# Optimization experiments

Hardware: AMD Instinct MI355X
Metric: run time of the kernel (lower is better)

The kernel has to match this reference:

```python
import jax, jax.numpy as jnp
import numpy as np

NUM_HEADS = 8
LN_EPS = 1e-5


def layer_norm(x, g, b):
    mu = jnp.mean(x, axis=-1, keepdims=True)
    var = jnp.mean(jnp.square(x - mu), axis=-1, keepdims=True)
    return (x - mu) / jnp.sqrt(var + LN_EPS) * g + b


def setup_inputs() -> dict:
    key = jax.random.key(0)
    ks = jax.random.split(key, 16)
    B, N, D, F = 16, 1024, 256, 1024
    s = 0.02
    return {
        "x": jax.random.normal(ks[0], (B, N, D), jnp.float32),
        "spatial_encoding": jax.random.normal(ks[1], (B, N, N), jnp.float32),
        "edge_encoding": jax.random.normal(ks[2], (B, N, N), jnp.float32),
        "gamma1": jnp.ones((D,), jnp.float32),
        "beta1": jnp.zeros((D,), jnp.float32),
        "gamma2": jnp.ones((D,), jnp.float32),
        "beta2": jnp.zeros((D,), jnp.float32),
        "Wq": jax.random.normal(ks[3], (D, D), jnp.float32) * s,
        "Wk": jax.random.normal(ks[4], (D, D), jnp.float32) * s,
        "Wv": jax.random.normal(ks[5], (D, D), jnp.float32) * s,
        "Wo": jax.random.normal(ks[6], (D, D), jnp.float32) * s,
        "W1": jax.random.normal(ks[7], (F, D), jnp.float32) * s,
        "b1": jnp.zeros((F,), jnp.float32),
        "W2": jax.random.normal(ks[8], (D, F), jnp.float32) * s,
        "b2": jnp.zeros((D,), jnp.float32),
    }


def reference(x, spatial_encoding, edge_encoding, gamma1, beta1, gamma2, beta2,
              Wq, Wk, Wv, Wo, W1, b1, W2, b2):
    B, N, D = x.shape
    H = NUM_HEADS
    hd = D // H
    scale = D ** (-0.5)  # source scales by hidden_dim, not head_size

    att_in = layer_norm(x, gamma1, beta1)

    def proj(W):  # [B,N,D] -> [B,H,N,hd]
        return (att_in @ W.T).reshape(B, N, H, hd).transpose(0, 2, 1, 3)

    q, k, v = proj(Wq), proj(Wk), proj(Wv)
    bias = (spatial_encoding + edge_encoding)[:, None]  # [B,1,N,N]
    a = jnp.einsum('bhnd,bhmd->bhnm', q, k) * scale + bias
    pad_mask = jnp.any(a != 0, axis=-1)  # [B,H,N]
    a = jnp.where(pad_mask[..., None], a, -jnp.inf)
    p = jnp.nan_to_num(jax.nn.softmax(a, axis=-1))
    o = jnp.einsum('bhnm,bhmd->bhnd', p, v)
    attn = o.transpose(0, 2, 1, 3).reshape(B, N, D) @ Wo.T
    att_output = attn + x

    pad_mask2 = jnp.any(att_output == 0, axis=-1)  # [B,N]
    ffn_in = layer_norm(x, gamma2, beta2)  # note: norm of x per the source
    h = jax.nn.gelu(ffn_in @ W1.T + b1, approximate=True)
    ffn_out = h @ W2.T + b2 + att_output
    return jnp.where(pad_mask2[..., None], 0.0, ffn_out)
```

## Files before the change

kernel.cpp:

```cpp
#include <hip/hip_runtime.h>
#include <hip/hip_bf16.h>
#include <math.h>

#define Bq 16
#define Nq 1024
#define Dq 256
#define Fq 1024
#define Hq 8
#define HDq 32
#define Mq (Bq * Nq)
#define SCALE 0.0625f
#define LN_EPS 1e-5f

typedef __attribute__((ext_vector_type(8))) short short8;
typedef __attribute__((ext_vector_type(4))) float f32x4;

__device__ __forceinline__ float bf2f(unsigned short s) {
    unsigned u = ((unsigned)s) << 16;
    return __builtin_bit_cast(float, u);
}
__device__ __forceinline__ unsigned short f2bf(float f) {
    __hip_bfloat16 h = __float2bfloat16(f);
    return __builtin_bit_cast(unsigned short, h);
}

typedef __attribute__((address_space(3))) unsigned int lds_uint;
typedef const __attribute__((address_space(1))) unsigned int glb_uint;
__device__ __forceinline__ void async16(void* lds, const void* g) {
    __builtin_amdgcn_global_load_lds((glb_uint*)g, (lds_uint*)lds, 16, 0, 0);
}

__device__ __forceinline__ float gelu_tanh(float v) {
    const float c = 0.7978845608028654f;
    float u = c * (v + 0.044715f * v * v * v);
    return 0.5f * v * (1.0f + tanhf(u));
}

__global__ __launch_bounds__(256) void cvt_weights(
    const float* __restrict__ Wq, const float* __restrict__ Wk,
    const float* __restrict__ Wv, const float* __restrict__ Wo,
    const float* __restrict__ W1, const float* __restrict__ W2,
    unsigned short* __restrict__ dst)
{
    const int blk = blockIdx.x;
    int seg, local;
    if (blk < 256)      { seg = blk >> 6; local = blk & 63; }
    else if (blk < 512) { seg = 4; local = blk - 256; }
    else                { seg = 5; local = blk - 512; }
    const float* srcs[6] = {Wq, Wk, Wv, Wo, W1, W2};
    const size_t dsto[6] = {0, 65536, 131072, 196608, 262144, 524288};
    const float* src = srcs[seg] + (size_t)local * 1024;
    unsigned short* d = dst + dsto[seg] + (size_t)local * 1024;
    const int t4 = threadIdx.x * 4;
    float4 v = *(const float4*)(src + t4);
    uint2 o;
    o.x = (unsigned)f2bf(v.x) | ((unsigned)f2bf(v.y) << 16);
    o.y = (unsigned)f2bf(v.z) | ((unsigned)f2bf(v.w) << 16);
    *(uint2*)(d + t4) = o;
}

__global__ __launch_bounds__(256) void ln2_kernel(
    const float* __restrict__ x,
    const float* __restrict__ g1, const float* __restrict__ bb1,
    const float* __restrict__ g2, const float* __restrict__ bb2,
    unsigned short* __restrict__ att_in, unsigned short* __restrict__ ffn_in)
{
    const int row = blockIdx.x;
    const int t = threadIdx.x;
    const size_t base = (size_t)row * Dq;
    float v = x[base + t];

    float s = v, sq = v * v;
    #pragma unroll
    for (int off = 32; off > 0; off >>= 1) {
        s  += __shfl_down(s, off);
        sq += __shfl_down(sq, off);
    }
    __shared__ float ssum[4], ssq[4];
    __shared__ float mu_s, rstd_s;
    const int lane = t & 63, wid = t >> 6;
    if (lane == 0) { ssum[wid] = s; ssq[wid] = sq; }
    __syncthreads();
    if (t == 0) {
        float S = ssum[0] + ssum[1] + ssum[2] + ssum[3];
        float Q = ssq[0] + ssq[1] + ssq[2] + ssq[3];
        float mu = S * (1.0f / Dq);
        float var = Q * (1.0f / Dq) - mu * mu;
        mu_s = mu;
        rstd_s = rsqrtf(var + LN_EPS);
    }
    __syncthreads();
    const float nx = (v - mu_s) * rstd_s;
    att_in[base + t] = f2bf(nx * g1[t] + bb1[t]);
    ffn_in[base + t] = f2bf(nx * g2[t] + bb2[t]);
}

#define TM 128
#define TN 128
#define TK 32

__global__ __launch_bounds__(256) void gemm_mfma(
    const unsigned short* __restrict__ A, const unsigned short* __restrict__ W,
    const float* __restrict__ bias, const float* __restrict__ add,
    float* __restrict__ outF, unsigned short* __restrict__ outBF,
    unsigned short* __restrict__ Qb, unsigned short* __restrict__ Kb,
    unsigned short* __restrict__ Vt,
    int M, int Nc, int K, int mode, int apply_gelu)
{
    __shared__ unsigned short As[TM * TK];
    __shared__ unsigned short Bs[TN * TK];
    const int t = threadIdx.x;
    const int w = t >> 6, lane = t & 63;
    const int col = lane & 15, quad = lane >> 4;
    const int wr = w >> 1, wc = w & 1;
    const int row0 = blockIdx.y * TM;
    const int col0 = blockIdx.x * TN;

    f32x4 acc[4][4] = {};

    for (int k0 = 0; k0 < K; k0 += TK) {
        #pragma unroll
        for (int j = 0; j < 2; j++) {
            const int c = w * 128 + j * 64 + lane;
            const int r = c >> 2, seg = c & 3;
            async16(&As[(size_t)(w * 128 + j * 64) * 8],
                    A + (size_t)(row0 + r) * K + k0 + seg * 8);
            async16(&Bs[(size_t)(w * 128 + j * 64) * 8],
                    W + (size_t)(col0 + r) * K + k0 + seg * 8);
        }
        __syncthreads();
        short8 wf[4], af[4];
        #pragma unroll
        for (int i = 0; i < 4; i++)
            wf[i] = *(const short8*)&Bs[(wc * 64 + i * 16 + col) * TK + quad * 8];
        #pragma unroll
        for (int j = 0; j < 4; j++)
            af[j] = *(const short8*)&As[(wr * 64 + j * 16 + col) * TK + quad * 8];
        #pragma unroll
        for (int i = 0; i < 4; i++)
            #pragma unroll
            for (int j = 0; j < 4; j++)
                acc[i][j] = __builtin_amdgcn_mfma_f32_16x16x32_bf16(wf[i], af[j], acc[i][j], 0, 0, 0);
        __syncthreads();
    }

    #pragma unroll
    for (int i = 0; i < 4; i++) {
        #pragma unroll
        for (int j = 0; j < 4; j++) {
            const int c0 = col0 + wc * 64 + i * 16 + quad * 4;
            const int r  = row0 + wr * 64 + j * 16 + col;
            float4 v = make_float4(acc[i][j][0], acc[i][j][1], acc[i][j][2], acc[i][j][3]);
            if (mode == 2 && c0 < 256) { v.x *= SCALE; v.y *= SCALE; v.z *= SCALE; v.w *= SCALE; }
            if (bias) {
                float4 bb = *(const float4*)&bias[c0];
                v.x += bb.x; v.y += bb.y; v.z += bb.z; v.w += bb.w;
            }
            if (apply_gelu) {
                v.x = gelu_tanh(v.x); v.y = gelu_tanh(v.y);
                v.z = gelu_tanh(v.z); v.w = gelu_tanh(v.w);
            }
            if (add) {
                float4 aa = *(const float4*)&add[(size_t)r * Nc + c0];
                v.x += aa.x; v.y += aa.y; v.z += aa.z; v.w += aa.w;
            }
            if (mode == 0) {
                *(float4*)&outF[(size_t)r * Nc + c0] = v;
            } else if (mode == 1) {
                uint2 o;
                o.x = (unsigned)f2bf(v.x) | ((unsigned)f2bf(v.y) << 16);
                o.y = (unsigned)f2bf(v.z) | ((unsigned)f2bf(v.w) << 16);
                *(uint2*)&outBF[(size_t)r * Nc + c0] = o;
            } else {
                const int b = r >> 10, n = r & 1023;
                if (c0 < 512) {
                    const int cq = c0 & 255;
                    const int h = cq >> 5, d0 = cq & 31;
                    unsigned short* dst = (c0 < 256 ? Qb : Kb);
                    uint2 o;
                    o.x = (unsigned)f2bf(v.x) | ((unsigned)f2bf(v.y) << 16);
                    o.y = (unsigned)f2bf(v.z) | ((unsigned)f2bf(v.w) << 16);
                    *(uint2*)&dst[(((size_t)(b * Hq + h) << 10) + n) * HDq + d0] = o;
                } else {
                    const int cv = c0 - 512;
                    const int h = cv >> 5, d0 = cv & 31;
                    unsigned short* dst = Vt + (((size_t)(b * Hq + h) * HDq + d0) << 10) + n;
                    dst[0]      = f2bf(v.x);
                    dst[1024]   = f2bf(v.y);
                    dst[2048]   = f2bf(v.z);
                    dst[3072]   = f2bf(v.w);
                }
            }
        }
    }
}

#define BSTR 1028

__global__ __launch_bounds__(512, 4) void attn_mfma(
    const unsigned short* __restrict__ Qbf, const unsigned short* __restrict__ Kbf,
    const unsigned short* __restrict__ Vt, const float* __restrict__ sp,
    const float* __restrict__ ed, unsigned short* __restrict__ O16)
{
    const int b = blockIdx.y;
    const int n0 = blockIdx.x * 16;
    const int t = threadIdx.x;
    const int h = t >> 6;
    const int lane = t & 63;
    const int col = lane & 15;
    const int quad = lane >> 4;

    __shared__ unsigned short bias16[16 * BSTR];
    __shared__ unsigned short S16[8][16 * 128];

    {
        const float* spb = sp + ((size_t)b * Nq + n0) * Nq;
        const float* edb = ed + ((size_t)b * Nq + n0) * Nq;
        for (int i = t; i < 4096; i += 512) {
            const int r = i >> 8;
            const int c4 = i & 255;
            float4 a = *(const float4*)(spb + (size_t)r * Nq + c4 * 4);
            float4 e = *(const float4*)(edb + (size_t)r * Nq + c4 * 4);
            uint2 o;
            o.x = (unsigned)f2bf(a.x + e.x) | ((unsigned)f2bf(a.y + e.y) << 16);
            o.y = (unsigned)f2bf(a.z + e.z) | ((unsigned)f2bf(a.w + e.w) << 16);
            *(uint2*)&bias16[r * BSTR + c4 * 4] = o;
        }
    }
    __syncthreads();

    const size_t hb = (size_t)b * Hq + h;
    const unsigned short* Qh = Qbf + hb * (Nq * HDq);
    const unsigned short* Kh = Kbf + hb * (Nq * HDq);
    const unsigned short* Vh = Vt  + hb * (HDq * Nq);
    unsigned short* Sw = &S16[h][0];

    const short8 aq = *(const short8*)(Qh + (size_t)(n0 + col) * HDq + quad * 8);

    f32x4 o0 = {0.f, 0.f, 0.f, 0.f}, o1 = {0.f, 0.f, 0.f, 0.f};
    float rsum[4] = {0.f, 0.f, 0.f, 0.f};

    for (int tt = 0; tt < 8; tt++) {
        const int k0 = tt * 128;
        #pragma unroll
        for (int m = 0; m < 8; m++) {
            const int m0 = k0 + m * 16;
            short8 bk = *(const short8*)(Kh + (size_t)(m0 + col) * HDq + quad * 8);
            f32x4 cc = {0.f, 0.f, 0.f, 0.f};
            cc = __builtin_amdgcn_mfma_f32_16x16x32_bf16(aq, bk, cc, 0, 0, 0);
            #pragma unroll
            for (int i = 0; i < 4; i++) {
                const int r = quad * 4 + i;
                float s = cc[i] + bf2f(bias16[r * BSTR + m0 + col]);
                float e = __expf(s);
                rsum[i] += e;
                const int sidx = (r * 128 + m * 16 + col) ^ ((r & 7) << 3);
                Sw[sidx] = f2bf(e);
            }
        }
        #pragma unroll
        for (int c = 0; c < 4; c++) {
            const int ridx = (col * 128 + c * 32 + quad * 8) ^ ((col & 7) << 3);
            short8 ap  = *(const short8*)&Sw[ridx];
            short8 bv0 = *(const short8*)(Vh + (size_t)col * Nq + k0 + c * 32 + quad * 8);
            short8 bv1 = *(const short8*)(Vh + (size_t)(col + 16) * Nq + k0 + c * 32 + quad * 8);
            o0 = __builtin_amdgcn_mfma_f32_16x16x32_bf16(ap, bv0, o0, 0, 0, 0);
            o1 = __builtin_amdgcn_mfma_f32_16x16x32_bf16(ap, bv1, o1, 0, 0, 0);
        }
    }

    #pragma unroll
    for (int off = 1; off < 16; off <<= 1) {
        #pragma unroll
        for (int i = 0; i < 4; i++) rsum[i] += __shfl_xor(rsum[i], off, 16);
    }

    unsigned short* op = O16 + ((size_t)b * Nq + n0) * Dq + h * HDq;
    #pragma unroll
    for (int i = 0; i < 4; i++) {
        const float inv = 1.0f / rsum[i];
        const int q = quad * 4 + i;
        op[(size_t)q * Dq + col]      = f2bf(o0[i] * inv);
        op[(size_t)q * Dq + col + 16] = f2bf(o1[i] * inv);
    }
}

__global__ __launch_bounds__(256) void pad2_kernel(
    const float* __restrict__ AO, float* __restrict__ out)
{
    const int row = blockIdx.x;
    const int t = threadIdx.x;
    const float v = AO[(size_t)row * Dq + t];
    unsigned long long m = __ballot(v == 0.0f);
    __shared__ unsigned long long w[4];
    if ((t & 63) == 0) w[t >> 6] = m;
    __syncthreads();
    if ((w[0] | w[1] | w[2] | w[3]) != 0ULL)
        out[(size_t)row * Dq + t] = 0.0f;
}

extern "C" void kernel_launch(void* const* d_in, const int* in_sizes, int n_in,
                              void* d_out, int out_size, void* d_ws, size_t ws_size,
                              hipStream_t stream)
{
    const float* x      = (const float*)d_in[0];
    const float* sp     = (const float*)d_in[1];
    const float* ed     = (const float*)d_in[2];
    const float* gamma1 = (const float*)d_in[3];
    const float* beta1  = (const float*)d_in[4];
    const float* gamma2 = (const float*)d_in[5];
    const float* beta2  = (const float*)d_in[6];
    const float* Wq     = (const float*)d_in[7];
    const float* Wk     = (const float*)d_in[8];
    const float* Wv     = (const float*)d_in[9];
    const float* Wo     = (const float*)d_in[10];
    const float* W1     = (const float*)d_in[11];
    const float* b1     = (const float*)d_in[12];
    const float* W2     = (const float*)d_in[13];
    const float* b2     = (const float*)d_in[14];
    float* out = (float*)d_out;

    unsigned short* s = (unsigned short*)d_ws;
    const size_t MD = (size_t)Mq * Dq;
    unsigned short* att_in16 = s;
    unsigned short* ffn_in16 = s + MD;
    unsigned short* Qbf      = s + 2 * MD;
    unsigned short* Kbf      = s + 3 * MD;
    unsigned short* Vtb      = s + 4 * MD;
    unsigned short* W16      = s + 5 * MD;
    unsigned short* h16      = s + 5 * MD + 786432;
    unsigned short* O16      = att_in16;
    float*          AO       = (float*)Qbf;

    unsigned short* Wo16 = W16 + 196608;
    unsigned short* W116 = W16 + 262144;
    unsigned short* W216 = W16 + 524288;

    cvt_weights<<<768, 256, 0, stream>>>(Wq, Wk, Wv, Wo, W1, W2, W16);

    ln2_kernel<<<Mq, 256, 0, stream>>>(x, gamma1, beta1, gamma2, beta2, att_in16, ffn_in16);

    dim3 gQKV(768 / TN, Mq / TM);
    gemm_mfma<<<gQKV, 256, 0, stream>>>(att_in16, W16, nullptr, nullptr, nullptr, nullptr,
                                        Qbf, Kbf, Vtb, Mq, 768, Dq, 2, 0);

    attn_mfma<<<dim3(Nq / 16, Bq), 512, 0, stream>>>(Qbf, Kbf, Vtb, sp, ed, O16);

    dim3 gP(Dq / TN, Mq / TM);
    gemm_mfma<<<gP, 256, 0, stream>>>(O16, Wo16, nullptr, x, AO, nullptr,
                                      nullptr, nullptr, nullptr, Mq, Dq, Dq, 0, 0);

    dim3 gF1(Fq / TN, Mq / TM);
    gemm_mfma<<<gF1, 256, 0, stream>>>(ffn_in16, W116, b1, nullptr, nullptr, h16,
                                       nullptr, nullptr, nullptr, Mq, Fq, Dq, 1, 1);

    gemm_mfma<<<gP, 256, 0, stream>>>(h16, W216, b2, AO, out, nullptr,
                                      nullptr, nullptr, nullptr, Mq, Dq, Fq, 0, 0);

    pad2_kernel<<<Mq, 256, 0, stream>>>(AO, out);
}
```

Before: 412.1 us.

## Precompute bf16 attention bias in separate kernel, read from global in attention

Moves the spatial+edge bias sum and bf16 conversion out of the attention kernel into a standalone elementwise kernel that writes a bf16 bias buffer, reusing the h16 workspace. The attention kernel drops its 32KB shared-memory bias tile and the barrier, reads bias directly from global memory per MFMA tile, and raises launch bounds to 8 blocks per CU. This aims to raise occupancy and overlap bias loads with compute. In exchange it adds a full extra write and read of a 32MB bf16 bias tensor and uses strided per-element global loads in the inner loop.

```diff
diff --git a/kernel.cpp b/kernel.cpp
--- a/kernel.cpp
+++ b/kernel.cpp
@@ -57,6 +57,23 @@
     o.x = (unsigned)f2bf(v.x) | ((unsigned)f2bf(v.y) << 16);
     o.y = (unsigned)f2bf(v.z) | ((unsigned)f2bf(v.w) << 16);
     *(uint2*)(d + t4) = o;
+}
+
+__global__ __launch_bounds__(256) void bias_cvt(
+    const float* __restrict__ sp, const float* __restrict__ ed,
+    unsigned short* __restrict__ dst)
+{
+    const size_t i = ((size_t)blockIdx.x * 256 + threadIdx.x) * 8;
+    float4 a0 = *(const float4*)(sp + i);
+    float4 a1 = *(const float4*)(sp + i + 4);
+    float4 e0 = *(const float4*)(ed + i);
+    float4 e1 = *(const float4*)(ed + i + 4);
+    uint4 o;
+    o.x = (unsigned)f2bf(a0.x + e0.x) | ((unsigned)f2bf(a0.y + e0.y) << 16);
+    o.y = (unsigned)f2bf(a0.z + e0.z) | ((unsigned)f2bf(a0.w + e0.w) << 16);
+    o.z = (unsigned)f2bf(a1.x + e1.x) | ((unsigned)f2bf(a1.y + e1.y) << 16);
+    o.w = (unsigned)f2bf(a1.z + e1.z) | ((unsigned)f2bf(a1.w + e1.w) << 16);
+    *(uint4*)(dst + i) = o;
 }
 
 __global__ __launch_bounds__(256) void ln2_kernel(
@@ -195,12 +212,10 @@
     }
 }
 
-#define BSTR 1028
-
-__global__ __launch_bounds__(512, 4) void attn_mfma(
+__global__ __launch_bounds__(512, 8) void attn_mfma(
     const unsigned short* __restrict__ Qbf, const unsigned short* __restrict__ Kbf,
-    const unsigned short* __restrict__ Vt, const float* __restrict__ sp,
-    const float* __restrict__ ed, unsigned short* __restrict__ O16)
+    const unsigned short* __restrict__ Vt, const unsigned short* __restrict__ biasg,
+    unsigned short* __restrict__ O16)
 {
     const int b = blockIdx.y;
     const int n0 = blockIdx.x * 16;
@@ -210,29 +225,13 @@
     const int col = lane & 15;
     const int quad = lane >> 4;
 
-    __shared__ unsigned short bias16[16 * BSTR];
     __shared__ unsigned short S16[8][16 * 128];
-
-    {
-        const float* spb = sp + ((size_t)b * Nq + n0) * Nq;
-        const float* edb = ed + ((size_t)b * Nq + n0) * Nq;
-        for (int i = t; i < 4096; i += 512) {
-            const int r = i >> 8;
-            const int c4 = i & 255;
-            float4 a = *(const float4*)(spb + (size_t)r * Nq + c4 * 4);
-            float4 e = *(const float4*)(edb + (size_t)r * Nq + c4 * 4);
-            uint2 o;
-            o.x = (unsigned)f2bf(a.x + e.x) | ((unsigned)f2bf(a.y + e.y) << 16);
-            o.y = (unsigned)f2bf(a.z + e.z) | ((unsigned)f2bf(a.w + e.w) << 16);
-            *(uint2*)&bias16[r * BSTR + c4 * 4] = o;
-        }
-    }
-    __syncthreads();
 
     const size_t hb = (size_t)b * Hq + h;
     const unsigned short* Qh = Qbf + hb * (Nq * HDq);
     const unsigned short* Kh = Kbf + hb * (Nq * HDq);
     const unsigned short* Vh = Vt  + hb * (HDq * Nq);
+    const unsigned short* bg = biasg + (((size_t)b * Nq + n0) << 10);
     unsigned short* Sw = &S16[h][0];
 
     const short8 aq = *(const short8*)(Qh + (size_t)(n0 + col) * HDq + quad * 8);
@@ -251,7 +250,7 @@
             #pragma unroll
             for (int i = 0; i < 4; i++) {
                 const int r = quad * 4 + i;
-                float s = cc[i] + bf2f(bias16[r * BSTR + m0 + col]);
+                float s = cc[i] + bf2f(bg[(size_t)r * Nq + m0 + col]);
                 float e = __expf(s);
                 rsum[i] += e;
                 const int sidx = (r * 128 + m * 16 + col) ^ ((r & 7) << 3);
@@ -331,6 +330,7 @@
     unsigned short* h16      = s + 5 * MD + 786432;
     unsigned short* O16      = att_in16;
     float*          AO       = (float*)Qbf;
+    unsigned short* bias16   = h16;
 
     unsigned short* Wo16 = W16 + 196608;
     unsigned short* W116 = W16 + 262144;
@@ -338,13 +338,15 @@
 
     cvt_weights<<<768, 256, 0, stream>>>(Wq, Wk, Wv, Wo, W1, W2, W16);
 
+    bias_cvt<<<8192, 256, 0, stream>>>(sp, ed, bias16);
+
     ln2_kernel<<<Mq, 256, 0, stream>>>(x, gamma1, beta1, gamma2, beta2, att_in16, ffn_in16);
 
     dim3 gQKV(768 / TN, Mq / TM);
     gemm_mfma<<<gQKV, 256, 0, stream>>>(att_in16, W16, nullptr, nullptr, nullptr, nullptr,
                                         Qbf, Kbf, Vtb, Mq, 768, Dq, 2, 0);
 
-    attn_mfma<<<dim3(Nq / 16, Bq), 512, 0, stream>>>(Qbf, Kbf, Vtb, sp, ed, O16);
+    attn_mfma<<<dim3(Nq / 16, Bq), 512, 0, stream>>>(Qbf, Kbf, Vtb, bias16, O16);
 
     dim3 gP(Dq / TN, Mq / TM);
     gemm_mfma<<<gP, 256, 0, stream>>>(O16, Wo16, nullptr, x, AO, nullptr,
```

After: 522.6 us. 1.27x slower.

## Precompute bf16 attention bias in MFMA fragment order in a separate kernel

Applied to the files above, without the earlier changes.

Moves the spatial+edge bias summation and bf16 conversion out of the attention kernel into a new pre-pass kernel. That pass writes the bias permuted into the exact per-lane MFMA output layout, so each attention lane loads its four bias values with one 8-byte read. This frees the 32KB bias LDS tile, raises the launch-bounds occupancy target, and remaps block indices with a swizzle. The cost is an extra kernel plus a 32MB bf16 write and reread of the bias, which reuses the h16 buffer region before the FFN overwrites it.

```diff
diff --git a/kernel.cpp b/kernel.cpp
--- a/kernel.cpp
+++ b/kernel.cpp
@@ -57,6 +57,44 @@
     o.x = (unsigned)f2bf(v.x) | ((unsigned)f2bf(v.y) << 16);
     o.y = (unsigned)f2bf(v.z) | ((unsigned)f2bf(v.w) << 16);
     *(uint2*)(d + t4) = o;
+}
+
+__global__ __launch_bounds__(256) void bias_cvt_perm(
+    const float* __restrict__ sp, const float* __restrict__ ed,
+    unsigned short* __restrict__ P)
+{
+    const int nt = blockIdx.x, b = blockIdx.y;
+    const int t = threadIdx.x;
+    __shared__ unsigned short lds[16][1032];
+    const size_t src0 = ((size_t)b * Nq + nt * 16) * Nq;
+
+    for (int idx = t; idx < 4096; idx += 256) {
+        const int r = idx >> 8, c4 = (idx & 255) * 4;
+        float4 a = *(const float4*)(sp + src0 + (size_t)r * Nq + c4);
+        float4 e = *(const float4*)(ed + src0 + (size_t)r * Nq + c4);
+        uint2 o;
+        o.x = (unsigned)f2bf(a.x + e.x) | ((unsigned)f2bf(a.y + e.y) << 16);
+        o.y = (unsigned)f2bf(a.z + e.z) | ((unsigned)f2bf(a.w + e.w) << 16);
+        *(uint2*)&lds[r][c4] = o;
+    }
+    __syncthreads();
+
+    unsigned short* Ps = P + ((size_t)(b * 64 + nt) << 14);
+    #pragma unroll
+    for (int it = 0; it < 8; it++) {
+        const int o   = (it * 256 + t) * 8;
+        const int r0  = o & 15;
+        const int col = (o >> 4) & 15;
+        const int m   = (o >> 8) & 7;
+        const int tt  = (o >> 11) & 7;
+        const int c   = tt * 128 + m * 16 + col;
+        uint4 w;
+        w.x = (unsigned)lds[r0 + 0][c] | ((unsigned)lds[r0 + 1][c] << 16);
+        w.y = (unsigned)lds[r0 + 2][c] | ((unsigned)lds[r0 + 3][c] << 16);
+        w.z = (unsigned)lds[r0 + 4][c] | ((unsigned)lds[r0 + 5][c] << 16);
+        w.w = (unsigned)lds[r0 + 6][c] | ((unsigned)lds[r0 + 7][c] << 16);
+        *(uint4*)(Ps + o) = w;
+    }
 }
 
 __global__ __launch_bounds__(256) void ln2_kernel(
@@ -195,44 +233,30 @@
     }
 }
 
-#define BSTR 1028
-
-__global__ __launch_bounds__(512, 4) void attn_mfma(
+__global__ __launch_bounds__(512, 8) void attn_mfma(
     const unsigned short* __restrict__ Qbf, const unsigned short* __restrict__ Kbf,
-    const unsigned short* __restrict__ Vt, const float* __restrict__ sp,
-    const float* __restrict__ ed, unsigned short* __restrict__ O16)
-{
-    const int b = blockIdx.y;
-    const int n0 = blockIdx.x * 16;
+    const unsigned short* __restrict__ Vt, const unsigned short* __restrict__ biasP,
+    unsigned short* __restrict__ O16)
+{
+    const int flat = blockIdx.y * gridDim.x + blockIdx.x;
+    const int id2  = (flat & 7) * 128 + (flat >> 3);
+    const int b    = id2 >> 6;
+    const int nt   = id2 & 63;
+    const int n0   = nt * 16;
+
     const int t = threadIdx.x;
     const int h = t >> 6;
     const int lane = t & 63;
     const int col = lane & 15;
     const int quad = lane >> 4;
 
-    __shared__ unsigned short bias16[16 * BSTR];
     __shared__ unsigned short S16[8][16 * 128];
-
-    {
-        const float* spb = sp + ((size_t)b * Nq + n0) * Nq;
-        const float* edb = ed + ((size_t)b * Nq + n0) * Nq;
-        for (int i = t; i < 4096; i += 512) {
-            const int r = i >> 8;
-            const int c4 = i & 255;
-            float4 a = *(const float4*)(spb + (size_t)r * Nq + c4 * 4);
-            float4 e = *(const float4*)(edb + (size_t)r * Nq + c4 * 4);
-            uint2 o;
-            o.x = (unsigned)f2bf(a.x + e.x) | ((unsigned)f2bf(a.y + e.y) << 16);
-            o.y = (unsigned)f2bf(a.z + e.z) | ((unsigned)f2bf(a.w + e.w) << 16);
-            *(uint2*)&bias16[r * BSTR + c4 * 4] = o;
-        }
-    }
-    __syncthreads();
 
     const size_t hb = (size_t)b * Hq + h;
     const unsigned short* Qh = Qbf + hb * (Nq * HDq);
     const unsigned short* Kh = Kbf + hb * (Nq * HDq);
     const unsigned short* Vh = Vt  + hb * (HDq * Nq);
+    const unsigned short* Ps = biasP + ((size_t)(b * 64 + nt) << 14);
     unsigned short* Sw = &S16[h][0];
 
     const short8 aq = *(const short8*)(Qh + (size_t)(n0 + col) * HDq + quad * 8);
@@ -246,12 +270,17 @@
         for (int m = 0; m < 8; m++) {
             const int m0 = k0 + m * 16;
             short8 bk = *(const short8*)(Kh + (size_t)(m0 + col) * HDq + quad * 8);
+            uint2 bv = *(const uint2*)(Ps + ((tt * 8 + m) << 8) + col * 16 + quad * 4);
             f32x4 cc = {0.f, 0.f, 0.f, 0.f};
             cc = __builtin_amdgcn_mfma_f32_16x16x32_bf16(aq, bk, cc, 0, 0, 0);
+            const float bi[4] = {
+                bf2f((unsigned short)(bv.x & 0xffff)), bf2f((unsigned short)(bv.x >> 16)),
+                bf2f((unsigned short)(bv.y & 0xffff)), bf2f((unsigned short)(bv.y >> 16))
+            };
             #pragma unroll
             for (int i = 0; i < 4; i++) {
                 const int r = quad * 4 + i;
-                float s = cc[i] + bf2f(bias16[r * BSTR + m0 + col]);
+                float s = cc[i] + bi[i];
                 float e = __expf(s);
                 rsum[i] += e;
                 const int sidx = (r * 128 + m * 16 + col) ^ ((r & 7) << 3);
@@ -331,6 +360,7 @@
     unsigned short* h16      = s + 5 * MD + 786432;
     unsigned short* O16      = att_in16;
     float*          AO       = (float*)Qbf;
+    unsigned short* biasP    = h16;
 
     unsigned short* Wo16 = W16 + 196608;
     unsigned short* W116 = W16 + 262144;
@@ -338,13 +368,15 @@
 
     cvt_weights<<<768, 256, 0, stream>>>(Wq, Wk, Wv, Wo, W1, W2, W16);
 
+    bias_cvt_perm<<<dim3(64, 16), 256, 0, stream>>>(sp, ed, biasP);
+
     ln2_kernel<<<Mq, 256, 0, stream>>>(x, gamma1, beta1, gamma2, beta2, att_in16, ffn_in16);
 
     dim3 gQKV(768 / TN, Mq / TM);
     gemm_mfma<<<gQKV, 256, 0, stream>>>(att_in16, W16, nullptr, nullptr, nullptr, nullptr,
                                         Qbf, Kbf, Vtb, Mq, 768, Dq, 2, 0);
 
-    attn_mfma<<<dim3(Nq / 16, Bq), 512, 0, stream>>>(Qbf, Kbf, Vtb, sp, ed, O16);
+    attn_mfma<<<dim3(Nq / 16, Bq), 512, 0, stream>>>(Qbf, Kbf, Vtb, biasP, O16);
 
     dim3 gP(Dq / TN, Mq / TM);
     gemm_mfma<<<gP, 256, 0, stream>>>(O16, Wo16, nullptr, x, AO, nullptr,
```

Measured after the change: 489.5 us. +18.8%, slower.
